# Kernel tuning notes

Hardware: AMD Instinct MI355X
Metric: run time of the kernel (lower is better)

Reference implementation:

```python
import jax, jax.numpy as jnp
import numpy as np

N_NODES = 50000


def gcn_conv(x, src, dst, W, b, n):
    # PyG GCNConv: h = x @ W; add self-loops; sym-norm aggregate; + bias
    h = x @ W
    loop = jnp.arange(n, dtype=src.dtype)
    s = jnp.concatenate([src, loop])
    d = jnp.concatenate([dst, loop])
    deg = jax.ops.segment_sum(jnp.ones(s.shape[0], h.dtype), d, num_segments=n)
    dinv = jnp.where(deg > 0, jax.lax.rsqrt(deg), 0.0)
    norm = dinv[s] * dinv[d]  # [E+n]
    msg = h[s] * norm[:, None]  # [E+n, C] gather
    out = jax.ops.segment_sum(msg, d, num_segments=n)  # scatter-add
    return out + b


def mlp_decode(z, src, dst, Wa, ba, Wb, bb):
    feat = jnp.concatenate([z[src], z[dst]], axis=1)  # [P, 2*out]
    hid = jax.nn.relu(feat @ Wa + ba)
    return hid @ Wb + bb  # [P, 1]


def setup_inputs() -> dict:
    key = jax.random.key(0)
    ks = jax.random.split(key, 12)
    in_c, hid_c, out_c = 128, 128, 64
    E, P = 800000, 200000
    x = jax.random.normal(ks[0], (N_NODES, in_c), dtype=jnp.float32)
    edge_index = jax.random.randint(ks[1], (2, E), 0, N_NODES, dtype=jnp.int64)
    pos_edge_index = jax.random.randint(ks[2], (2, P), 0, N_NODES, dtype=jnp.int64)
    neg_edge_index = jax.random.randint(ks[3], (2, P), 0, N_NODES, dtype=jnp.int64)
    s1 = 1.0 / np.sqrt(in_c)
    s2 = 1.0 / np.sqrt(hid_c)
    s3 = 1.0 / np.sqrt(2 * out_c)
    W1 = jax.random.uniform(ks[4], (in_c, hid_c), jnp.float32, -s1, s1)
    b1 = jnp.zeros((hid_c,), jnp.float32)
    W2 = jax.random.uniform(ks[5], (hid_c, out_c), jnp.float32, -s2, s2)
    b2 = jnp.zeros((out_c,), jnp.float32)
    Wa = jax.random.uniform(ks[6], (2 * out_c, hid_c), jnp.float32, -s3, s3)
    ba = jax.random.uniform(ks[7], (hid_c,), jnp.float32, -s3, s3)
    Wb = jax.random.uniform(ks[8], (hid_c, 1), jnp.float32, -s2, s2)
    bb = jax.random.uniform(ks[9], (1,), jnp.float32, -s2, s2)
    return {"x": x, "edge_index": edge_index, "pos_edge_index": pos_edge_index,
            "neg_edge_index": neg_edge_index, "W1": W1, "b1": b1, "W2": W2,
            "b2": b2, "Wa": Wa, "ba": ba, "Wb": Wb, "bb": bb}


def reference(x, edge_index, pos_edge_index, neg_edge_index,
              W1, b1, W2, b2, Wa, ba, Wb, bb):
    src, dst = edge_index[0], edge_index[1]
    n = x.shape[0]
    z = gcn_conv(x, src, dst, W1, b1, n)
    z = jax.nn.relu(z)  # dropout disabled in eval mode
    z = gcn_conv(z, src, dst, W2, b2, n)
    pos_pred = mlp_decode(z, pos_edge_index[0], pos_edge_index[1], Wa, ba, Wb, bb)
    neg_pred = mlp_decode(z, neg_edge_index[0], neg_edge_index[1], Wa, ba, Wb, bb)
    return (pos_pred, neg_pred)
```

## Files before the change

### kernel.cpp

```cpp
#include <hip/hip_runtime.h>
#include <hip/hip_bf16.h>
#include <hip/hip_fp16.h>

#define NODES 50000
#define NEDGE 800000
#define NPRED 200000

typedef __attribute__((ext_vector_type(8))) short bf16x8;
typedef __attribute__((ext_vector_type(8))) unsigned short u16x8;
typedef __attribute__((ext_vector_type(4))) float f32x4;

__device__ inline float bf2f(unsigned short u) {
    union { unsigned int i; float f; } v; v.i = ((unsigned int)u) << 16; return v.f;
}
__device__ inline unsigned short f2bf(float f) {
    __hip_bfloat16 b = __float2bfloat16(f);
    return *(unsigned short*)&b;
}

#define RANK_BLOCKS 782
__global__ __launch_bounds__(256) void rank_perm(const int* __restrict__ dstv, int* __restrict__ cnt,
                                                 int* __restrict__ rank, int E4,
                                                 const float* __restrict__ W1, const float* __restrict__ W2,
                                                 const float* __restrict__ Wa,
                                                 unsigned short* __restrict__ pW1,
                                                 unsigned short* __restrict__ pW2,
                                                 unsigned short* __restrict__ pWa) {
    if (blockIdx.x < RANK_BLOCKS) {
        int i = blockIdx.x * 256 + threadIdx.x;
        if (i < E4) {
            int4 d4 = ((const int4*)dstv)[i];
            int4 r4;
            r4.x = atomicAdd(&cnt[d4.x], 1);
            r4.y = atomicAdd(&cnt[d4.y], 1);
            r4.z = atomicAdd(&cnt[d4.z], 1);
            r4.w = atomicAdd(&cnt[d4.w], 1);
            ((int4*)rank)[i] = r4;
        }
        return;
    }
    int t = (blockIdx.x - RANK_BLOCKS) * 256 + threadIdx.x;
    if (t >= 5120) return;
    const float* W; unsigned short* P; int N;
    if (t < 2048)      { W = W1; P = pW1; N = 128; }
    else if (t < 3072) { W = W2; P = pW2; N = 64;  t -= 2048; }
    else               { W = Wa; P = pWa; N = 128; t -= 3072; }
    int lane = t & 63;
    int kt = (t >> 6) & 3;
    int nt = t >> 8;
    int n = nt * 16 + (lane & 15);
    int k0 = kt * 32 + (lane >> 4) * 8;
#pragma unroll
    for (int j = 0; j < 8; ++j) P[t * 8 + j] = f2bf(W[(k0 + j) * N + n]);
}

__global__ __launch_bounds__(256) void scan_bsum(const int* __restrict__ cnt, int* __restrict__ bsum, int n) {
    __shared__ int s[256];
    int t = threadIdx.x, b = blockIdx.x;
    int base = b * 1024 + t * 4;
    int sum = 0;
#pragma unroll
    for (int j = 0; j < 4; ++j) { int i = base + j; if (i < n) sum += cnt[i]; }
    s[t] = sum; __syncthreads();
    for (int off = 128; off >= 1; off >>= 1) {
        if (t < off) s[t] += s[t + off];
        __syncthreads();
    }
    if (t == 0) bsum[b] = s[0];
}

__global__ void scan_boff(const int* __restrict__ bsum, int* __restrict__ boff, int nb,
                          int* __restrict__ row_ptr, int n) {
    int t = threadIdx.x;
    int v = (t < nb) ? bsum[t] : 0;
    int orig = v;
    for (int off = 1; off < 64; off <<= 1) {
        int u = __shfl_up(v, off, 64);
        if (t >= off) v += u;
    }
    boff[t] = v - orig;
    if (t == 63) row_ptr[n] = v;
}

__global__ __launch_bounds__(256) void scan_write(const int* __restrict__ cnt, const int* __restrict__ boff,
                                                  int* __restrict__ row_ptr, float* __restrict__ dinv,
                                                  int* __restrict__ hist, int* __restrict__ rank2, int n) {
    __shared__ int s[256];
    __shared__ int lh[64], lbase[64];
    int t = threadIdx.x, b = blockIdx.x;
    if (t < 64) lh[t] = 0;
    int base = b * 1024 + t * 4;
    int v[4]; int sum = 0;
#pragma unroll
    for (int j = 0; j < 4; ++j) { int i = base + j; v[j] = (i < n) ? cnt[i] : 0; sum += v[j]; }
    s[t] = sum; __syncthreads();
    for (int off = 1; off < 256; off <<= 1) {
        int u = (t >= off) ? s[t - off] : 0;
        __syncthreads();
        s[t] += u;
        __syncthreads();
    }
    int run = s[t] - sum + boff[b];
    int lr[4], bin[4];
#pragma unroll
    for (int j = 0; j < 4; ++j) {
        int i = base + j;
        if (i < n) {
            row_ptr[i] = run; run += v[j];
            dinv[i] = rsqrtf((float)(v[j] + 1));
            bin[j] = v[j] < 63 ? v[j] : 63;
            lr[j] = atomicAdd(&lh[bin[j]], 1);
        }
    }
    __syncthreads();
    if (t < 64) lbase[t] = atomicAdd(&hist[t], lh[t]);
    __syncthreads();
#pragma unroll
    for (int j = 0; j < 4; ++j) {
        int i = base + j;
        if (i < n) rank2[i] = lbase[bin[j]] + lr[j];
    }
}

__global__ void scan_hist(int* __restrict__ hist) {
    int t = threadIdx.x;
    int v = hist[t];
    int orig = v;
    for (int off = 1; off < 64; off <<= 1) {
        int u = __shfl_up(v, off, 64);
        if (t >= off) v += u;
    }
    hist[t] = v - orig;
}

__global__ __launch_bounds__(256) void scatter_order(const int* __restrict__ cnt, const int* __restrict__ rank2,
                                                     const int* __restrict__ hist, int* __restrict__ order, int n) {
    int i = blockIdx.x * 256 + threadIdx.x;
    if (i < n) {
        int d = cnt[i] < 63 ? cnt[i] : 63;
        order[hist[d] + rank2[i]] = i;
    }
}

__global__ __launch_bounds__(256) void csr_fill2(const int* __restrict__ ei, const int* __restrict__ rank,
                                                 const int* __restrict__ row_ptr, int* __restrict__ colv, int E4) {
    int i = blockIdx.x * 256 + threadIdx.x;
    if (i < E4) {
        int4 s4 = ((const int4*)ei)[i];
        int4 d4 = ((const int4*)(ei + NEDGE))[i];
        int4 r4 = ((const int4*)rank)[i];
        colv[row_ptr[d4.x] + r4.x] = s4.x;
        colv[row_ptr[d4.y] + r4.y] = s4.y;
        colv[row_ptr[d4.z] + r4.z] = s4.z;
        colv[row_ptr[d4.w] + r4.w] = s4.w;
    }
}

template <int NT, bool AFP32>
__global__ __launch_bounds__(256) void gemm_mfma(const void* __restrict__ Xv,
                                                 const unsigned short* __restrict__ perm,
                                                 unsigned short* __restrict__ H, int M) {
    int w = blockIdx.x * 4 + (threadIdx.x >> 6);
    int m0 = w * 16;
    if (m0 >= M) return;
    int lane = threadIdx.x & 63;
    int m = lane & 15, q = lane >> 4;
    size_t row = (size_t)(m0 + m);
    bf16x8 a[4];
    if (AFP32) {
        const float* X = (const float*)Xv;
#pragma unroll
        for (int kt = 0; kt < 4; ++kt) {
            float4 f0 = *(const float4*)&X[row * 128 + kt * 32 + q * 8];
            float4 f1 = *(const float4*)&X[row * 128 + kt * 32 + q * 8 + 4];
            bf16x8 av;
            av[0] = (short)f2bf(f0.x); av[1] = (short)f2bf(f0.y);
            av[2] = (short)f2bf(f0.z); av[3] = (short)f2bf(f0.w);
            av[4] = (short)f2bf(f1.x); av[5] = (short)f2bf(f1.y);
            av[6] = (short)f2bf(f1.z); av[7] = (short)f2bf(f1.w);
            a[kt] = av;
        }
    } else {
        const unsigned short* X = (const unsigned short*)Xv;
#pragma unroll
        for (int kt = 0; kt < 4; ++kt)
            a[kt] = *(const bf16x8*)&X[row * 128 + kt * 32 + q * 8];
    }
    const int N = NT * 16;
#pragma unroll
    for (int nt = 0; nt < NT; ++nt) {
        f32x4 c = {0.f, 0.f, 0.f, 0.f};
#pragma unroll
        for (int kt = 0; kt < 4; ++kt) {
            bf16x8 b = *(const bf16x8*)(perm + (size_t)((nt * 4 + kt) * 64 + lane) * 8);
            c = __builtin_amdgcn_mfma_f32_16x16x32_bf16(a[kt], b, c, 0, 0, 0);
        }
#pragma unroll
        for (int r = 0; r < 4; ++r)
            H[(size_t)(m0 + q * 4 + r) * N + nt * 16 + m] = f2bf(c[r]);
    }
}

template <int C, bool RELU>
__global__ __launch_bounds__(256) void agg_bf16(const unsigned short* __restrict__ h,
                                                const int* __restrict__ row_ptr, const int* __restrict__ colv,
                                                const float* __restrict__ dinv, const float* __restrict__ bias,
                                                const int* __restrict__ order,
                                                unsigned short* __restrict__ out) {
    constexpr int TPN = C / 8;
    constexpr int NPB = 256 / TPN;
    int g = blockIdx.x * NPB + threadIdx.x / TPN;
    if (g >= NODES) return;
    int d = order[g];
    int c8 = (threadIdx.x % TPN) * 8;
    float dv = dinv[d];
    float acc[8];
    u16x8 self = *(const u16x8*)&h[(size_t)d * C + c8];
#pragma unroll
    for (int j = 0; j < 8; ++j) acc[j] = bf2f(self[j]) * dv;
    int i = row_ptr[d], end = row_ptr[d + 1];
    for (; i + 7 < end; i += 8) {
        int s[8]; float w[8]; u16x8 r[8];
#pragma unroll
        for (int k = 0; k < 8; ++k) s[k] = colv[i + k];
#pragma unroll
        for (int k = 0; k < 8; ++k) w[k] = dinv[s[k]];
#pragma unroll
        for (int k = 0; k < 8; ++k) r[k] = *(const u16x8*)&h[(size_t)s[k] * C + c8];
#pragma unroll
        for (int k = 0; k < 8; ++k)
#pragma unroll
            for (int j = 0; j < 8; ++j) acc[j] += bf2f(r[k][j]) * w[k];
    }
    for (; i + 3 < end; i += 4) {
        int s[4]; float w[4]; u16x8 r[4];
#pragma unroll
        for (int k = 0; k < 4; ++k) s[k] = colv[i + k];
#pragma unroll
        for (int k = 0; k < 4; ++k) w[k] = dinv[s[k]];
#pragma unroll
        for (int k = 0; k < 4; ++k) r[k] = *(const u16x8*)&h[(size_t)s[k] * C + c8];
#pragma unroll
        for (int k = 0; k < 4; ++k)
#pragma unroll
            for (int j = 0; j < 8; ++j) acc[j] += bf2f(r[k][j]) * w[k];
    }
    for (; i < end; ++i) {
        int s0 = colv[i];
        float w0 = dinv[s0];
        u16x8 r0 = *(const u16x8*)&h[(size_t)s0 * C + c8];
#pragma unroll
        for (int j = 0; j < 8; ++j) acc[j] += bf2f(r0[j]) * w0;
    }
    u16x8 ov;
#pragma unroll
    for (int j = 0; j < 8; ++j) {
        float o = acc[j] * dv + bias[c8 + j];
        if (RELU) o = fmaxf(o, 0.f);
        ov[j] = f2bf(o);
    }
    *(u16x8*)&out[(size_t)d * C + c8] = ov;
}

__global__ __launch_bounds__(256) void decode_mfma4(const unsigned short* __restrict__ zb,
                                                    const int* __restrict__ pos, const int* __restrict__ neg,
                                                    const unsigned short* __restrict__ perm,
                                                    const float* __restrict__ ba, const float* __restrict__ Wb,
                                                    const float* __restrict__ bb, float* __restrict__ out, int P) {
    __shared__ unsigned short sB[2048 * 8];
    int tid = threadIdx.x;
#pragma unroll
    for (int i = tid * 8; i < 2048 * 8; i += 256 * 8)
        *(u16x8*)&sB[i] = *(const u16x8*)&perm[i];
    __syncthreads();

    int w = blockIdx.x * 4 + (tid >> 6);
    if (w >= 3125) return;
    int lane = tid & 63;
    int m = lane & 15, q = lane >> 4;
    float bav[8], wbv[8];
#pragma unroll
    for (int nt = 0; nt < 8; ++nt) { bav[nt] = ba[nt * 16 + m]; wbv[nt] = Wb[nt * 16 + m]; }
    float bbv = bb[0];
    int g0 = w * 4;

    int idxS[3][2], idxD[3][2], base[3];
    bf16x8 A[2][8];
    auto loadIdx = [&](int it) {
        int slot = it % 3;
        int g = g0 + it;
        int half = (g >= 6250) ? 1 : 0;
        const int* src = half ? neg : pos;
        int e0 = (g - half * 6250) * 32;
        base[slot] = half * P + e0;
        idxS[slot][0] = src[e0 + m];      idxD[slot][0] = src[P + e0 + m];
        idxS[slot][1] = src[e0 + 16 + m]; idxD[slot][1] = src[P + e0 + 16 + m];
    };
    auto loadA = [&](int it) {
        int slot = it % 3, buf = it & 1;
        size_t s0 = (size_t)idxS[slot][0] * 64, d0 = (size_t)idxD[slot][0] * 64;
        size_t s1 = (size_t)idxS[slot][1] * 64, d1 = (size_t)idxD[slot][1] * 64;
        A[buf][0] = *(const bf16x8*)(zb + s0 + q * 8);
        A[buf][1] = *(const bf16x8*)(zb + s0 + 32 + q * 8);
        A[buf][2] = *(const bf16x8*)(zb + d0 + q * 8);
        A[buf][3] = *(const bf16x8*)(zb + d0 + 32 + q * 8);
        A[buf][4] = *(const bf16x8*)(zb + s1 + q * 8);
        A[buf][5] = *(const bf16x8*)(zb + s1 + 32 + q * 8);
        A[buf][6] = *(const bf16x8*)(zb + d1 + q * 8);
        A[buf][7] = *(const bf16x8*)(zb + d1 + 32 + q * 8);
    };

    loadIdx(0); loadIdx(1); loadA(0);
#pragma unroll
    for (int it = 0; it < 4; ++it) {
        if (it + 2 < 4) loadIdx(it + 2);
        if (it + 1 < 4) loadA(it + 1);
        int buf = it & 1;
        float p0[4] = {0.f, 0.f, 0.f, 0.f};
        float p1[4] = {0.f, 0.f, 0.f, 0.f};
#pragma unroll
        for (int nt = 0; nt < 8; ++nt) {
            bf16x8 b0 = *(const bf16x8*)&sB[(size_t)((nt * 4 + 0) * 64 + lane) * 8];
            bf16x8 b1 = *(const bf16x8*)&sB[(size_t)((nt * 4 + 1) * 64 + lane) * 8];
            bf16x8 b2 = *(const bf16x8*)&sB[(size_t)((nt * 4 + 2) * 64 + lane) * 8];
            bf16x8 b3 = *(const bf16x8*)&sB[(size_t)((nt * 4 + 3) * 64 + lane) * 8];
            f32x4 c0a = {0.f, 0.f, 0.f, 0.f}, c0b = {0.f, 0.f, 0.f, 0.f};
            f32x4 c1a = {0.f, 0.f, 0.f, 0.f}, c1b = {0.f, 0.f, 0.f, 0.f};
            c0a = __builtin_amdgcn_mfma_f32_16x16x32_bf16(A[buf][0], b0, c0a, 0, 0, 0);
            c1a = __builtin_amdgcn_mfma_f32_16x16x32_bf16(A[buf][4], b0, c1a, 0, 0, 0);
            c0b = __builtin_amdgcn_mfma_f32_16x16x32_bf16(A[buf][2], b2, c0b, 0, 0, 0);
            c1b = __builtin_amdgcn_mfma_f32_16x16x32_bf16(A[buf][6], b2, c1b, 0, 0, 0);
            c0a = __builtin_amdgcn_mfma_f32_16x16x32_bf16(A[buf][1], b1, c0a, 0, 0, 0);
            c1a = __builtin_amdgcn_mfma_f32_16x16x32_bf16(A[buf][5], b1, c1a, 0, 0, 0);
            c0b = __builtin_amdgcn_mfma_f32_16x16x32_bf16(A[buf][3], b3, c0b, 0, 0, 0);
            c1b = __builtin_amdgcn_mfma_f32_16x16x32_bf16(A[buf][7], b3, c1b, 0, 0, 0);
#pragma unroll
            for (int r = 0; r < 4; ++r) {
                p0[r] += fmaxf(c0a[r] + c0b[r] + bav[nt], 0.f) * wbv[nt];
                p1[r] += fmaxf(c1a[r] + c1b[r] + bav[nt], 0.f) * wbv[nt];
            }
        }
#pragma unroll
        for (int off = 1; off <= 8; off <<= 1) {
#pragma unroll
            for (int r = 0; r < 4; ++r) {
                p0[r] += __shfl_xor(p0[r], off, 64);
                p1[r] += __shfl_xor(p1[r], off, 64);
            }
        }
        if (m == 0) {
            int slot = it % 3;
            float4 st0 = { p0[0] + bbv, p0[1] + bbv, p0[2] + bbv, p0[3] + bbv };
            float4 st1 = { p1[0] + bbv, p1[1] + bbv, p1[2] + bbv, p1[3] + bbv };
            *(float4*)&out[base[slot] + q * 4] = st0;
            *(float4*)&out[base[slot] + 16 + q * 4] = st1;
        }
    }
}

extern "C" void kernel_launch(void* const* d_in, const int* in_sizes, int n_in,
                              void* d_out, int out_size, void* d_ws, size_t ws_size,
                              hipStream_t stream) {
    const int N = NODES, E = NEDGE, P = NPRED;
    const float* x  = (const float*)d_in[0];
    const int*   ei = (const int*)d_in[1];
    const int*  pos = (const int*)d_in[2];
    const int*  neg = (const int*)d_in[3];
    const float* W1 = (const float*)d_in[4];
    const float* b1 = (const float*)d_in[5];
    const float* W2 = (const float*)d_in[6];
    const float* b2 = (const float*)d_in[7];
    const float* Wa = (const float*)d_in[8];
    const float* ba = (const float*)d_in[9];
    const float* Wb = (const float*)d_in[10];
    const float* bb = (const float*)d_in[11];
    float* out = (float*)d_out;

    char* w = (char*)d_ws;
    auto alloc = [&](size_t bytes) { char* p = w; w += (bytes + 255) & ~(size_t)255; return p; };
    int*   cnt     = (int*)alloc((size_t)(N + 64) * 4);
    int*   hist    = cnt + N;
    int*   rankb   = (int*)alloc((size_t)E * 4);
    int*   rank2   = (int*)alloc((size_t)N * 4);
    int*   order   = (int*)alloc((size_t)N * 4);
    int*   row_ptr = (int*)alloc((size_t)(N + 1) * 4);
    int*   colv    = (int*)alloc((size_t)E * 4);
    float* dinv    = (float*)alloc((size_t)N * 4);
    int*   bsum    = (int*)alloc(64 * 4);
    int*   boff    = (int*)alloc(64 * 4);
    unsigned short* h1b = (unsigned short*)alloc((size_t)N * 128 * 2);
    unsigned short* z1b = (unsigned short*)alloc((size_t)N * 128 * 2);
    unsigned short* h2b = (unsigned short*)alloc((size_t)N * 64 * 2);
    unsigned short* zb  = (unsigned short*)alloc((size_t)N * 64 * 2);
    unsigned short* pW1 = (unsigned short*)alloc(2048 * 8 * 2);
    unsigned short* pW2 = (unsigned short*)alloc(1024 * 8 * 2);
    unsigned short* pWa = (unsigned short*)alloc(2048 * 8 * 2);

    const int nb = (N + 1023) / 1024;
    hipMemsetAsync(cnt, 0, (size_t)(N + 64) * 4, stream);
    rank_perm<<<RANK_BLOCKS + 20, 256, 0, stream>>>(ei + E, cnt, rankb, E / 4,
                                                    W1, W2, Wa, pW1, pW2, pWa);
    scan_bsum<<<nb, 256, 0, stream>>>(cnt, bsum, N);
    scan_boff<<<1, 64, 0, stream>>>(bsum, boff, nb, row_ptr, N);
    scan_write<<<nb, 256, 0, stream>>>(cnt, boff, row_ptr, dinv, hist, rank2, N);
    scan_hist<<<1, 64, 0, stream>>>(hist);
    scatter_order<<<(N + 255) / 256, 256, 0, stream>>>(cnt, rank2, hist, order, N);
    csr_fill2<<<(E / 4 + 255) / 256, 256, 0, stream>>>(ei, rankb, row_ptr, colv, E / 4);

    gemm_mfma<8, true><<<782, 256, 0, stream>>>(x, pW1, h1b, N);
    agg_bf16<128, true><<<N / 16, 256, 0, stream>>>(h1b, row_ptr, colv, dinv, b1, order, z1b);

    gemm_mfma<4, false><<<782, 256, 0, stream>>>(z1b, pW2, h2b, N);
    agg_bf16<64, false><<<(N + 31) / 32, 256, 0, stream>>>(h2b, row_ptr, colv, dinv, b2, order, zb);

    decode_mfma4<<<782, 256, 0, stream>>>(zb, pos, neg, pWa, ba, Wb, bb, out, P);
}
```

Measured before the change: 248.5 us.

## Drop degree-sorted node order, fuse scan kernels, merge CSR fill with first GEMM

Removes the degree-binned node reordering (histogram, hist scan, scatter_order), so aggregation processes nodes in natural index order. Folds the block-offset scan into scan_write2 via wave reductions, and launches CSR fill and the first GEMM in one kernel split by block index. The decoder now handles 8 groups per wave instead of 4, with half as many blocks and a clamp for the tail. The aim is fewer launches and less setup work, at the cost of losing load balancing by degree in the aggregation kernels and lower decoder occupancy.

```diff
diff --git a/kernel.cpp b/kernel.cpp
--- a/kernel.cpp
+++ b/kernel.cpp
@@ -69,26 +69,22 @@
     if (t == 0) bsum[b] = s[0];
 }
 
-__global__ void scan_boff(const int* __restrict__ bsum, int* __restrict__ boff, int nb,
-                          int* __restrict__ row_ptr, int n) {
-    int t = threadIdx.x;
-    int v = (t < nb) ? bsum[t] : 0;
-    int orig = v;
-    for (int off = 1; off < 64; off <<= 1) {
-        int u = __shfl_up(v, off, 64);
-        if (t >= off) v += u;
-    }
-    boff[t] = v - orig;
-    if (t == 63) row_ptr[n] = v;
-}
-
-__global__ __launch_bounds__(256) void scan_write(const int* __restrict__ cnt, const int* __restrict__ boff,
-                                                  int* __restrict__ row_ptr, float* __restrict__ dinv,
-                                                  int* __restrict__ hist, int* __restrict__ rank2, int n) {
+__global__ __launch_bounds__(256) void scan_write2(const int* __restrict__ cnt, const int* __restrict__ bsum,
+                                                   int* __restrict__ row_ptr, float* __restrict__ dinv,
+                                                   int n, int nb) {
     __shared__ int s[256];
-    __shared__ int lh[64], lbase[64];
+    __shared__ int sboff;
     int t = threadIdx.x, b = blockIdx.x;
-    if (t < 64) lh[t] = 0;
+    if (t < 64) {
+        int v  = (t < nb) ? bsum[t] : 0;
+        int vp = (t < b) ? v : 0;
+#pragma unroll
+        for (int off = 1; off < 64; off <<= 1) {
+            vp += __shfl_xor(vp, off, 64);
+            v  += __shfl_xor(v, off, 64);
+        }
+        if (t == 0) { sboff = vp; if (b == 0) row_ptr[n] = v; }
+    }
     int base = b * 1024 + t * 4;
     int v[4]; int sum = 0;
 #pragma unroll
@@ -100,64 +96,70 @@
         s[t] += u;
         __syncthreads();
     }
-    int run = s[t] - sum + boff[b];
-    int lr[4], bin[4];
+    int run = s[t] - sum + sboff;
 #pragma unroll
     for (int j = 0; j < 4; ++j) {
         int i = base + j;
         if (i < n) {
             row_ptr[i] = run; run += v[j];
             dinv[i] = rsqrtf((float)(v[j] + 1));
-            bin[j] = v[j] < 63 ? v[j] : 63;
-            lr[j] = atomicAdd(&lh[bin[j]], 1);
-        }
-    }
-    __syncthreads();
-    if (t < 64) lbase[t] = atomicAdd(&hist[t], lh[t]);
-    __syncthreads();
-#pragma unroll
-    for (int j = 0; j < 4; ++j) {
-        int i = base + j;
-        if (i < n) rank2[i] = lbase[bin[j]] + lr[j];
-    }
-}
-
-__global__ void scan_hist(int* __restrict__ hist) {
-    int t = threadIdx.x;
-    int v = hist[t];
-    int orig = v;
-    for (int off = 1; off < 64; off <<= 1) {
-        int u = __shfl_up(v, off, 64);
-        if (t >= off) v += u;
-    }
-    hist[t] = v - orig;
-}
-
-__global__ __launch_bounds__(256) void scatter_order(const int* __restrict__ cnt, const int* __restrict__ rank2,
-                                                     const int* __restrict__ hist, int* __restrict__ order, int n) {
-    int i = blockIdx.x * 256 + threadIdx.x;
-    if (i < n) {
-        int d = cnt[i] < 63 ? cnt[i] : 63;
-        order[hist[d] + rank2[i]] = i;
-    }
-}
-
-__global__ __launch_bounds__(256) void csr_fill2(const int* __restrict__ ei, const int* __restrict__ rank,
-                                                 const int* __restrict__ row_ptr, int* __restrict__ colv, int E4) {
-    int i = blockIdx.x * 256 + threadIdx.x;
-    if (i < E4) {
-        int4 s4 = ((const int4*)ei)[i];
-        int4 d4 = ((const int4*)(ei + NEDGE))[i];
-        int4 r4 = ((const int4*)rank)[i];
-        colv[row_ptr[d4.x] + r4.x] = s4.x;
-        colv[row_ptr[d4.y] + r4.y] = s4.y;
-        colv[row_ptr[d4.z] + r4.z] = s4.z;
-        colv[row_ptr[d4.w] + r4.w] = s4.w;
-    }
-}
-
-template <int NT, bool AFP32>
-__global__ __launch_bounds__(256) void gemm_mfma(const void* __restrict__ Xv,
+        }
+    }
+}
+
+#define FILL_BLOCKS 782
+__global__ __launch_bounds__(256) void fill_gemm1(const int* __restrict__ ei, const int* __restrict__ rank,
+                                                  const int* __restrict__ row_ptr, int* __restrict__ colv, int E4,
+                                                  const float* __restrict__ X,
+                                                  const unsigned short* __restrict__ pW1,
+                                                  unsigned short* __restrict__ H, int M) {
+    if (blockIdx.x < FILL_BLOCKS) {
+        int i = blockIdx.x * 256 + threadIdx.x;
+        if (i < E4) {
+            int4 s4 = ((const int4*)ei)[i];
+            int4 d4 = ((const int4*)(ei + NEDGE))[i];
+            int4 r4 = ((const int4*)rank)[i];
+            colv[row_ptr[d4.x] + r4.x] = s4.x;
+            colv[row_ptr[d4.y] + r4.y] = s4.y;
+            colv[row_ptr[d4.z] + r4.z] = s4.z;
+            colv[row_ptr[d4.w] + r4.w] = s4.w;
+        }
+        return;
+    }
+    int w = (blockIdx.x - FILL_BLOCKS) * 4 + (threadIdx.x >> 6);
+    int m0 = w * 16;
+    if (m0 >= M) return;
+    int lane = threadIdx.x & 63;
+    int m = lane & 15, q = lane >> 4;
+    size_t row = (size_t)(m0 + m);
+    bf16x8 a[4];
+#pragma unroll
+    for (int kt = 0; kt < 4; ++kt) {
+        float4 f0 = *(const float4*)&X[row * 128 + kt * 32 + q * 8];
+        float4 f1 = *(const float4*)&X[row * 128 + kt * 32 + q * 8 + 4];
+        bf16x8 av;
+        av[0] = (short)f2bf(f0.x); av[1] = (short)f2bf(f0.y);
+        av[2] = (short)f2bf(f0.z); av[3] = (short)f2bf(f0.w);
+        av[4] = (short)f2bf(f1.x); av[5] = (short)f2bf(f1.y);
+        av[6] = (short)f2bf(f1.z); av[7] = (short)f2bf(f1.w);
+        a[kt] = av;
+    }
+#pragma unroll
+    for (int nt = 0; nt < 8; ++nt) {
+        f32x4 c = {0.f, 0.f, 0.f, 0.f};
+#pragma unroll
+        for (int kt = 0; kt < 4; ++kt) {
+            bf16x8 b = *(const bf16x8*)(pW1 + (size_t)((nt * 4 + kt) * 64 + lane) * 8);
+            c = __builtin_amdgcn_mfma_f32_16x16x32_bf16(a[kt], b, c, 0, 0, 0);
+        }
+#pragma unroll
+        for (int r = 0; r < 4; ++r)
+            H[(size_t)(m0 + q * 4 + r) * 128 + nt * 16 + m] = f2bf(c[r]);
+    }
+}
+
+template <int NT>
+__global__ __launch_bounds__(256) void gemm_mfma(const unsigned short* __restrict__ X,
                                                  const unsigned short* __restrict__ perm,
                                                  unsigned short* __restrict__ H, int M) {
     int w = blockIdx.x * 4 + (threadIdx.x >> 6);
@@ -167,25 +169,9 @@
     int m = lane & 15, q = lane >> 4;
     size_t row = (size_t)(m0 + m);
     bf16x8 a[4];
-    if (AFP32) {
-        const float* X = (const float*)Xv;
-#pragma unroll
-        for (int kt = 0; kt < 4; ++kt) {
-            float4 f0 = *(const float4*)&X[row * 128 + kt * 32 + q * 8];
-            float4 f1 = *(const float4*)&X[row * 128 + kt * 32 + q * 8 + 4];
-            bf16x8 av;
-            av[0] = (short)f2bf(f0.x); av[1] = (short)f2bf(f0.y);
-            av[2] = (short)f2bf(f0.z); av[3] = (short)f2bf(f0.w);
-            av[4] = (short)f2bf(f1.x); av[5] = (short)f2bf(f1.y);
-            av[6] = (short)f2bf(f1.z); av[7] = (short)f2bf(f1.w);
-            a[kt] = av;
-        }
-    } else {
-        const unsigned short* X = (const unsigned short*)Xv;
-#pragma unroll
-        for (int kt = 0; kt < 4; ++kt)
-            a[kt] = *(const bf16x8*)&X[row * 128 + kt * 32 + q * 8];
-    }
+#pragma unroll
+    for (int kt = 0; kt < 4; ++kt)
+        a[kt] = *(const bf16x8*)&X[row * 128 + kt * 32 + q * 8];
     const int N = NT * 16;
 #pragma unroll
     for (int nt = 0; nt < NT; ++nt) {
@@ -205,13 +191,11 @@
 __global__ __launch_bounds__(256) void agg_bf16(const unsigned short* __restrict__ h,
                                                 const int* __restrict__ row_ptr, const int* __restrict__ colv,
                                                 const float* __restrict__ dinv, const float* __restrict__ bias,
-                                                const int* __restrict__ order,
                                                 unsigned short* __restrict__ out) {
     constexpr int TPN = C / 8;
     constexpr int NPB = 256 / TPN;
-    int g = blockIdx.x * NPB + threadIdx.x / TPN;
-    if (g >= NODES) return;
-    int d = order[g];
+    int d = blockIdx.x * NPB + threadIdx.x / TPN;
+    if (d >= NODES) return;
     int c8 = (threadIdx.x % TPN) * 8;
     float dv = dinv[d];
     float acc[8];
@@ -262,7 +246,7 @@
     *(u16x8*)&out[(size_t)d * C + c8] = ov;
 }
 
-__global__ __launch_bounds__(256) void decode_mfma4(const unsigned short* __restrict__ zb,
+__global__ __launch_bounds__(256) void decode_mfma5(const unsigned short* __restrict__ zb,
                                                     const int* __restrict__ pos, const int* __restrict__ neg,
                                                     const unsigned short* __restrict__ perm,
                                                     const float* __restrict__ ba, const float* __restrict__ Wb,
@@ -275,20 +259,20 @@
     __syncthreads();
 
     int w = blockIdx.x * 4 + (tid >> 6);
-    if (w >= 3125) return;
+    if (w >= 1563) return;
     int lane = tid & 63;
     int m = lane & 15, q = lane >> 4;
     float bav[8], wbv[8];
 #pragma unroll
     for (int nt = 0; nt < 8; ++nt) { bav[nt] = ba[nt * 16 + m]; wbv[nt] = Wb[nt * 16 + m]; }
     float bbv = bb[0];
-    int g0 = w * 4;
+    int g0 = w * 8;
 
     int idxS[3][2], idxD[3][2], base[3];
     bf16x8 A[2][8];
     auto loadIdx = [&](int it) {
         int slot = it % 3;
-        int g = g0 + it;
+        int g = g0 + it; if (g > 12499) g = 12499;
         int half = (g >= 6250) ? 1 : 0;
         const int* src = half ? neg : pos;
         int e0 = (g - half * 6250) * 32;
@@ -312,9 +296,9 @@
 
     loadIdx(0); loadIdx(1); loadA(0);
 #pragma unroll
-    for (int it = 0; it < 4; ++it) {
-        if (it + 2 < 4) loadIdx(it + 2);
-        if (it + 1 < 4) loadA(it + 1);
+    for (int it = 0; it < 8; ++it) {
+        if (it + 2 < 8) loadIdx(it + 2);
+        if (it + 1 < 8) loadA(it + 1);
         int buf = it & 1;
         float p0[4] = {0.f, 0.f, 0.f, 0.f};
         float p1[4] = {0.f, 0.f, 0.f, 0.f};
@@ -378,16 +362,12 @@
 
     char* w = (char*)d_ws;
     auto alloc = [&](size_t bytes) { char* p = w; w += (bytes + 255) & ~(size_t)255; return p; };
-    int*   cnt     = (int*)alloc((size_t)(N + 64) * 4);
-    int*   hist    = cnt + N;
+    int*   cnt     = (int*)alloc((size_t)N * 4);
     int*   rankb   = (int*)alloc((size_t)E * 4);
-    int*   rank2   = (int*)alloc((size_t)N * 4);
-    int*   order   = (int*)alloc((size_t)N * 4);
     int*   row_ptr = (int*)alloc((size_t)(N + 1) * 4);
     int*   colv    = (int*)alloc((size_t)E * 4);
     float* dinv    = (float*)alloc((size_t)N * 4);
     int*   bsum    = (int*)alloc(64 * 4);
-    int*   boff    = (int*)alloc(64 * 4);
     unsigned short* h1b = (unsigned short*)alloc((size_t)N * 128 * 2);
     unsigned short* z1b = (unsigned short*)alloc((size_t)N * 128 * 2);
     unsigned short* h2b = (unsigned short*)alloc((size_t)N * 64 * 2);
@@ -397,21 +377,19 @@
     unsigned short* pWa = (unsigned short*)alloc(2048 * 8 * 2);
 
     const int nb = (N + 1023) / 1024;
-    hipMemsetAsync(cnt, 0, (size_t)(N + 64) * 4, stream);
+    hipMemsetAsync(cnt, 0, (size_t)N * 4, stream);
     rank_perm<<<RANK_BLOCKS + 20, 256, 0, stream>>>(ei + E, cnt, rankb, E / 4,
                                                     W1, W2, Wa, pW1, pW2, pWa);
     scan_bsum<<<nb, 256, 0, stream>>>(cnt, bsum, N);
-    scan_boff<<<1, 64, 0, stream>>>(bsum, boff, nb, row_ptr, N);
-    scan_write<<<nb, 256, 0, stream>>>(cnt, boff, row_ptr, dinv, hist, rank2, N);
-    scan_hist<<<1, 64, 0, stream>>>(hist);
-    scatter_order<<<(N + 255) / 256, 256, 0, stream>>>(cnt, rank2, hist, order, N);
-    csr_fill2<<<(E / 4 + 255) / 256, 256, 0, stream>>>(ei, rankb, row_ptr, colv, E / 4);
-
-    gemm_mfma<8, true><<<782, 256, 0, stream>>>(x, pW1, h1b, N);
-    agg_bf16<128, true><<<N / 16, 256, 0, stream>>>(h1b, row_ptr, colv, dinv, b1, order, z1b);
-
-    gemm_mfma<4, false><<<782, 256, 0, stream>>>(z1b, pW2, h2b, N);
-    agg_bf16<64, false><<<(N + 31) / 32, 256, 0, stream>>>(h2b, row_ptr, colv, dinv, b2, order, zb);
-
-    decode_mfma4<<<782, 256, 0, stream>>>(zb, pos, neg, pWa, ba, Wb, bb, out, P);
-}
+    scan_write2<<<nb, 256, 0, stream>>>(cnt, bsum, row_ptr, dinv, N, nb);
+
+    fill_gemm1<<<FILL_BLOCKS + 782, 256, 0, stream>>>(ei, rankb, row_ptr, colv, E / 4,
+                                                      x, pW1, h1b, N);
+
+    agg_bf16<128, true><<<N / 16, 256, 0, stream>>>(h1b, row_ptr, colv, dinv, b1, z1b);
+
+    gemm_mfma<4><<<782, 256, 0, stream>>>(z1b, pW2, h2b, N);
+    agg_bf16<64, false><<<(N + 31) / 32, 256, 0, stream>>>(h2b, row_ptr, colv, dinv, b2, zb);
+
+    decode_mfma5<<<391, 256, 0, stream>>>(zb, pos, neg, pWa, ba, Wb, bb, out, P);
+}
```

Result: faster. 241.2 us (-2.9%).
